# Kernel optimization log

Hardware: AMD Instinct MI355X
Metric: run time of the kernel (lower is better)

Reference implementation:

```python
import jax, jax.numpy as jnp
import numpy as np

B, H, S, D = 1, 16, 2048, 64


def setup_inputs() -> dict:
    key = jax.random.key(0)
    kq, kk, kv, km = jax.random.split(key, 4)
    q = jax.random.normal(kq, (B, H, S, D), dtype=jnp.float32)
    k = jax.random.normal(kk, (B, H, S, D), dtype=jnp.float32)
    v = jax.random.normal(kv, (B, H, S, D), dtype=jnp.float32)
    omask = jax.random.uniform(km, (B, H, S, S), dtype=jnp.float32)
    return {"q": q, "k": k, "v": v, "omask": omask}


def reference(q, k, v, omask):
    # mask = omask / sqrt(rowsum(omask)), nan -> 0
    row_sum = jnp.sum(omask, axis=-1, keepdims=True)  # [B,H,S,1]
    decay_mask = jnp.nan_to_num(omask / jnp.sqrt(row_sum), nan=0.0)
    # retention = (q k^T) * mask  -> [B,H,S,S]
    retention = jnp.einsum("bhsd,bhtd->bhst", q, k) * decay_mask
    # normalize by |rowsum(retention)| clamped to >= 1 (detached in original)
    scale = jnp.clip(jnp.abs(jnp.sum(retention, axis=-1, keepdims=True)), 1.0, None)
    retention = retention / scale
    # output = retention @ v -> [B,H,S,D]
    return jnp.einsum("bhst,bhtd->bhsd", retention, v)
```

## Files before the change

kernel.cpp:

```cpp
#include <hip/hip_runtime.h>

#define H 16
#define S 2048
#define D 64
#define BM 64
#define BN 64
#define NT (S / BN)
#define KP 72

typedef __attribute__((ext_vector_type(8))) short bf16x8;
typedef __attribute__((ext_vector_type(4))) short short4v;
typedef __attribute__((ext_vector_type(4))) float fx4;

static __device__ __forceinline__ short f2bf(float x) {
    unsigned u = __float_as_uint(x);
    u += 0x7fffu + ((u >> 16) & 1u);
    return (short)(u >> 16);
}
static __device__ __forceinline__ float bf2f(short s) {
    return __uint_as_float(((unsigned)(unsigned short)s) << 16);
}

__global__ __launch_bounds__(256)
void ParallelRetention_origin_25374666785438_kernel(
    const float* __restrict__ q, const float* __restrict__ k,
    const float* __restrict__ v, const float* __restrict__ om,
    float* __restrict__ out)
{
    __shared__ short ldsKh[2][BN * KP];
    __shared__ short ldsKl[2][BN * KP];
    __shared__ short ldsVT[2][BN * KP];
    __shared__ short ldsP[4 * 16 * KP];

    const int tid  = threadIdx.x;
    const int wave = tid >> 6;
    const int lane = tid & 63;
    const int col  = lane & 15;
    const int quad = lane >> 4;
    const int t_base = (tid >> 4) << 2;
    const int d4     = (tid & 15) << 2;

    const int h  = blockIdx.x & 15;
    const int qb = blockIdx.x >> 4;
    const int row0 = qb * BM;

    const size_t headQK = (size_t)h * S * D;
    const size_t headM  = (size_t)h * S * S;

    bf16x8 qh[2], qlo[2];
    {
        const int s_row = row0 + wave * 16 + col;
        const float* qp = q + headQK + (size_t)s_row * D + quad * 8;
#pragma unroll
        for (int c = 0; c < 2; ++c) {
            fx4 a = *(const fx4*)(qp + c * 32);
            fx4 b = *(const fx4*)(qp + c * 32 + 4);
            float f[8] = {a[0],a[1],a[2],a[3],b[0],b[1],b[2],b[3]};
#pragma unroll
            for (int j = 0; j < 8; ++j) {
                short hi = f2bf(f[j]);
                qh[c][j]  = hi;
                qlo[c][j] = f2bf(f[j] - bf2f(hi));
            }
        }
    }

    fx4 U[4];
#pragma unroll
    for (int nt = 0; nt < 4; ++nt) { U[nt][0]=0.f; U[nt][1]=0.f; U[nt][2]=0.f; U[nt][3]=0.f; }
    float rs_acc[4] = {0.f, 0.f, 0.f, 0.f};
    float T_acc[4]  = {0.f, 0.f, 0.f, 0.f};
    float om0[16], om1[16];

    const float* kbase0 = k + headQK;
    const float* vbase0 = v + headQK;
    const float* ombase = om + headM + (size_t)(row0 + wave * 16) * S;

    auto load_kv = [&](int t0, fx4 (&kr)[4], fx4 (&vr)[4]) {
        const float* kb = kbase0 + (size_t)t0 * D;
        const float* vb = vbase0 + (size_t)t0 * D;
#pragma unroll
        for (int r = 0; r < 4; ++r) {
            kr[r] = *(const fx4*)(kb + (size_t)(t_base + r) * D + d4);
            vr[r] = *(const fx4*)(vb + (size_t)(t_base + r) * D + d4);
        }
    };
    auto load_om = [&](int t0, float (&o)[16]) {
        const float* omp = ombase + t0;
#pragma unroll
        for (int tn = 0; tn < 4; ++tn)
#pragma unroll
            for (int r = 0; r < 4; ++r)
                o[tn * 4 + r] = omp[(size_t)(quad * 4 + r) * S + tn * 16 + col];
    };
    auto stage_write = [&](const fx4 (&kr)[4], const fx4 (&vr)[4],
                           short* Kh, short* Kl, short* VT) {
#pragma unroll
        for (int r = 0; r < 4; ++r) {
            short4v h4, l4;
#pragma unroll
            for (int j = 0; j < 4; ++j) {
                short hi = f2bf(kr[r][j]);
                h4[j] = hi;
                l4[j] = f2bf(kr[r][j] - bf2f(hi));
            }
            *(short4v*)(&Kh[(t_base + r) * KP + d4]) = h4;
            *(short4v*)(&Kl[(t_base + r) * KP + d4]) = l4;
        }
#pragma unroll
        for (int j = 0; j < 4; ++j) {
            short4v p;
#pragma unroll
            for (int r = 0; r < 4; ++r) p[r] = f2bf(vr[r][j]);
            *(short4v*)(&VT[(d4 + j) * KP + t_base]) = p;
        }
    };
    auto compute = [&](const short* Kh, const short* Kl, const short* VT,
                       const float (&omc)[16]) {
#pragma unroll
        for (int tn = 0; tn < 4; ++tn) {
            const short* kph = &Kh[(tn * 16 + col) * KP + quad * 8];
            const short* kpl = &Kl[(tn * 16 + col) * KP + quad * 8];
            bf16x8 kh0 = *(const bf16x8*)(kph);
            bf16x8 kh1 = *(const bf16x8*)(kph + 32);
            bf16x8 kl0 = *(const bf16x8*)(kpl);
            bf16x8 kl1 = *(const bf16x8*)(kpl + 32);
            fx4 z; z[0]=0.f; z[1]=0.f; z[2]=0.f; z[3]=0.f;
            z = __builtin_amdgcn_mfma_f32_16x16x32_bf16(qh[0],  kh0, z, 0, 0, 0);
            z = __builtin_amdgcn_mfma_f32_16x16x32_bf16(qh[1],  kh1, z, 0, 0, 0);
            z = __builtin_amdgcn_mfma_f32_16x16x32_bf16(qh[0],  kl0, z, 0, 0, 0);
            z = __builtin_amdgcn_mfma_f32_16x16x32_bf16(qh[1],  kl1, z, 0, 0, 0);
            z = __builtin_amdgcn_mfma_f32_16x16x32_bf16(qlo[0], kh0, z, 0, 0, 0);
            z = __builtin_amdgcn_mfma_f32_16x16x32_bf16(qlo[1], kh1, z, 0, 0, 0);
#pragma unroll
            for (int r = 0; r < 4; ++r) {
                float m = omc[tn * 4 + r];
                float p = z[r] * m;
                rs_acc[r] += m;
                T_acc[r]  += p;
                ldsP[(wave * 16 + quad * 4 + r) * KP + tn * 16 + col] = f2bf(p);
            }
        }
#pragma unroll
        for (int kt = 0; kt < 2; ++kt) {
            bf16x8 pa = *(const bf16x8*)(&ldsP[(wave * 16 + col) * KP + kt * 32 + quad * 8]);
#pragma unroll
            for (int nt = 0; nt < 4; ++nt) {
                bf16x8 vb = *(const bf16x8*)(&VT[(nt * 16 + col) * KP + kt * 32 + quad * 8]);
                U[nt] = __builtin_amdgcn_mfma_f32_16x16x32_bf16(pa, vb, U[nt], 0, 0, 0);
            }
        }
    };

    {
        fx4 kr[4], vr[4];
        load_kv(0, kr, vr);
        load_om(0, om0);
        stage_write(kr, vr, ldsKh[0], ldsKl[0], ldsVT[0]);
    }

    for (int it2 = 0; it2 < NT; it2 += 2) {
        {
            __syncthreads();
            fx4 kr[4], vr[4];
            load_kv((it2 + 1) * BN, kr, vr);
            load_om((it2 + 1) * BN, om1);
            compute(ldsKh[0], ldsKl[0], ldsVT[0], om0);
            stage_write(kr, vr, ldsKh[1], ldsKl[1], ldsVT[1]);
        }
        {
            __syncthreads();
            const bool pf = (it2 + 2 < NT);
            fx4 kr[4], vr[4];
            if (pf) {
                load_kv((it2 + 2) * BN, kr, vr);
                load_om((it2 + 2) * BN, om0);
            }
            compute(ldsKh[1], ldsKl[1], ldsVT[1], om1);
            if (pf) stage_write(kr, vr, ldsKh[0], ldsKl[0], ldsVT[0]);
        }
    }

#pragma unroll
    for (int off = 1; off < 16; off <<= 1) {
#pragma unroll
        for (int r = 0; r < 4; ++r) {
            rs_acc[r] += __shfl_xor(rs_acc[r], off, 64);
            T_acc[r]  += __shfl_xor(T_acc[r], off, 64);
        }
    }
    float factor[4];
#pragma unroll
    for (int r = 0; r < 4; ++r) {
        float rs  = rs_acc[r];
        float inv = rs > 0.f ? rsqrtf(rs) : 0.f;
        float rowsum = T_acc[r] * inv;
        float sc = fabsf(rowsum);
        sc = sc < 1.f ? 1.f : sc;
        factor[r] = inv / sc;
    }
    float* op = out + headQK + (size_t)(row0 + wave * 16) * D;
#pragma unroll
    for (int r = 0; r < 4; ++r)
#pragma unroll
        for (int nt = 0; nt < 4; ++nt)
            op[(size_t)(quad * 4 + r) * D + nt * 16 + col] = U[nt][r] * factor[r];
}

extern "C" void kernel_launch(void* const* d_in, const int* in_sizes, int n_in,
                              void* d_out, int out_size, void* d_ws, size_t ws_size,
                              hipStream_t stream) {
    const float* q  = (const float*)d_in[0];
    const float* k  = (const float*)d_in[1];
    const float* v  = (const float*)d_in[2];
    const float* om = (const float*)d_in[3];
    float* out = (float*)d_out;
    (void)in_sizes; (void)n_in; (void)out_size; (void)d_ws; (void)ws_size;

    dim3 grid(H * (S / BM));
    dim3 block(256);
    hipLaunchKernelGGL(ParallelRetention_origin_25374666785438_kernel,
                       grid, block, 0, stream, q, k, v, om, out);
}
```

Before: 408.8 us.

## Precompute bf16 K split and transposed V once, stage via direct global-to-LDS loads

Adds a prep kernel that converts K into bf16 hi/lo parts and V into a transposed bf16 layout in workspace, once per head. The main kernel then stages these tiles straight into swizzled LDS with global_load_lds, so each of the 32 query blocks per head no longer repeats the conversion. It also swaps MFMA operand order so the omask loads become contiguous fx4 vectors and row reductions become per-lane scalars, and it requests two blocks per CU. The cost is an extra launch and workspace traffic, plus XOR-swizzled LDS indexing that has to be correct.

Measured after the change: 394.7 us. 1.04x faster.

```diff
diff --git a/kernel.cpp b/kernel.cpp
--- a/kernel.cpp
+++ b/kernel.cpp
@@ -6,7 +6,6 @@
 #define BM 64
 #define BN 64
 #define NT (S / BN)
-#define KP 72
 
 typedef __attribute__((ext_vector_type(8))) short bf16x8;
 typedef __attribute__((ext_vector_type(4))) short short4v;
@@ -20,25 +19,83 @@
 static __device__ __forceinline__ float bf2f(short s) {
     return __uint_as_float(((unsigned)(unsigned short)s) << 16);
 }
+static __device__ __forceinline__ void gl_lds16(const void* g, void* l) {
+    __builtin_amdgcn_global_load_lds(
+        (const __attribute__((address_space(1))) unsigned int*)g,
+        (__attribute__((address_space(3))) unsigned int*)l, 16, 0, 0);
+}
 
 __global__ __launch_bounds__(256)
+void ParallelRetention_prep_kernel(
+    const float* __restrict__ k, const float* __restrict__ v,
+    short* __restrict__ khi, short* __restrict__ klo, short* __restrict__ vt)
+{
+    __shared__ short lv[64 * 72];
+    const int tid = threadIdx.x;
+    const int h  = blockIdx.x & 15;
+    const int sb = blockIdx.x >> 4;
+    const int s0 = sb * 64;
+    const int t_base = (tid >> 4) << 2;
+    const int d4     = (tid & 15) << 2;
+    const size_t hoff = (size_t)h * S * D;
+
+    {
+        const float* kb = k + hoff + (size_t)(s0 + t_base) * D + d4;
+#pragma unroll
+        for (int r = 0; r < 4; ++r) {
+            fx4 kr = *(const fx4*)(kb + (size_t)r * D);
+            short4v h4, l4;
+#pragma unroll
+            for (int j = 0; j < 4; ++j) {
+                short hi = f2bf(kr[j]);
+                h4[j] = hi;
+                l4[j] = f2bf(kr[j] - bf2f(hi));
+            }
+            *(short4v*)(&khi[hoff + (size_t)(s0 + t_base + r) * D + d4]) = h4;
+            *(short4v*)(&klo[hoff + (size_t)(s0 + t_base + r) * D + d4]) = l4;
+        }
+    }
+    {
+        const float* vb = v + hoff + (size_t)(s0 + t_base) * D + d4;
+        fx4 vr[4];
+#pragma unroll
+        for (int r = 0; r < 4; ++r) vr[r] = *(const fx4*)(vb + (size_t)r * D);
+#pragma unroll
+        for (int j = 0; j < 4; ++j) {
+            short4v p;
+#pragma unroll
+            for (int r = 0; r < 4; ++r) p[r] = f2bf(vr[r][j]);
+            *(short4v*)(&lv[(d4 + j) * 72 + t_base]) = p;
+        }
+    }
+    __syncthreads();
+    {
+        const int d = tid >> 2;
+        const int c = tid & 3;
+        bf16x8 a = *(const bf16x8*)(&lv[d * 72 + c * 16]);
+        bf16x8 b = *(const bf16x8*)(&lv[d * 72 + c * 16 + 8]);
+        short* o = vt + (size_t)h * D * S + (size_t)d * S + s0 + c * 16;
+        *(bf16x8*)(o)     = a;
+        *(bf16x8*)(o + 8) = b;
+    }
+}
+
+__global__ __launch_bounds__(256, 2)
 void ParallelRetention_origin_25374666785438_kernel(
-    const float* __restrict__ q, const float* __restrict__ k,
-    const float* __restrict__ v, const float* __restrict__ om,
-    float* __restrict__ out)
+    const float* __restrict__ q, const float* __restrict__ om,
+    const short* __restrict__ khi, const short* __restrict__ klo,
+    const short* __restrict__ vt, float* __restrict__ out)
 {
-    __shared__ short ldsKh[2][BN * KP];
-    __shared__ short ldsKl[2][BN * KP];
-    __shared__ short ldsVT[2][BN * KP];
-    __shared__ short ldsP[4 * 16 * KP];
+    __shared__ short ldsKh[2][64 * 64];
+    __shared__ short ldsKl[2][64 * 64];
+    __shared__ short ldsVT[2][64 * 64];
+    __shared__ short ldsP[64 * 64];
 
     const int tid  = threadIdx.x;
     const int wave = tid >> 6;
     const int lane = tid & 63;
     const int col  = lane & 15;
     const int quad = lane >> 4;
-    const int t_base = (tid >> 4) << 2;
-    const int d4     = (tid & 15) << 2;
 
     const int h  = blockIdx.x & 15;
     const int qb = blockIdx.x >> 4;
@@ -68,143 +125,120 @@
     fx4 U[4];
 #pragma unroll
     for (int nt = 0; nt < 4; ++nt) { U[nt][0]=0.f; U[nt][1]=0.f; U[nt][2]=0.f; U[nt][3]=0.f; }
-    float rs_acc[4] = {0.f, 0.f, 0.f, 0.f};
-    float T_acc[4]  = {0.f, 0.f, 0.f, 0.f};
-    float om0[16], om1[16];
-
-    const float* kbase0 = k + headQK;
-    const float* vbase0 = v + headQK;
-    const float* ombase = om + headM + (size_t)(row0 + wave * 16) * S;
-
-    auto load_kv = [&](int t0, fx4 (&kr)[4], fx4 (&vr)[4]) {
-        const float* kb = kbase0 + (size_t)t0 * D;
-        const float* vb = vbase0 + (size_t)t0 * D;
-#pragma unroll
-        for (int r = 0; r < 4; ++r) {
-            kr[r] = *(const fx4*)(kb + (size_t)(t_base + r) * D + d4);
-            vr[r] = *(const fx4*)(vb + (size_t)(t_base + r) * D + d4);
+    float rs_acc = 0.f, T_acc = 0.f;
+
+    const int xq   = quad ^ (col & 3);
+    const int cx   = (col >> 2) & 1;
+    const int rdC0 = col * 64 + xq * 8 + cx * 32;
+    const int rdC1 = col * 64 + xq * 8 + (cx ^ 1) * 32;
+    const int prow   = wave * 16 + col;
+    const int pwBase = prow * 64 + (quad & 1) * 4 + (((quad >> 1) ^ (col & 1))) * 8;
+    const int pxor   = (col >> 1) & 3;
+    const int prC0   = prow * 64 + xq * 8 + cx * 32;
+    const int prC1   = prow * 64 + xq * 8 + (cx ^ 1) * 32;
+    const int rowl = lane >> 3;
+    const int swz8 = ((lane & 7) ^ rowl) * 8;
+    const int kSrcOff = rowl * 64 + swz8;
+    const int vSrcOff = rowl * 2048 + swz8;
+
+    const short* khiH = khi + headQK;
+    const short* kloH = klo + headQK;
+    const short* vtH  = vt + (size_t)h * D * S;
+    const float* omp0 = om + headM + (size_t)(row0 + wave * 16 + col) * S + quad * 4;
+
+    auto stage = [&](int t0, short* dKh, short* dKl, short* dVT) {
+        const short* ks = khiH + (size_t)t0 * 64 + kSrcOff;
+        const short* ls = kloH + (size_t)t0 * 64 + kSrcOff;
+        const short* vs = vtH + t0 + vSrcOff;
+#pragma unroll
+        for (int c = 0; c < 6; ++c) {
+            int id = wave * 6 + c;
+            int j  = id & 7;
+            int tile = id >> 3;
+            if (tile == 0)      gl_lds16(ks + j * 512, dKh + j * 512);
+            else if (tile == 1) gl_lds16(ls + j * 512, dKl + j * 512);
+            else                gl_lds16(vs + (size_t)j * 8 * 2048, dVT + j * 512);
         }
     };
-    auto load_om = [&](int t0, float (&o)[16]) {
-        const float* omp = ombase + t0;
+    auto load_om = [&](int t0, fx4 (&o)[4]) {
 #pragma unroll
         for (int tn = 0; tn < 4; ++tn)
-#pragma unroll
-            for (int r = 0; r < 4; ++r)
-                o[tn * 4 + r] = omp[(size_t)(quad * 4 + r) * S + tn * 16 + col];
-    };
-    auto stage_write = [&](const fx4 (&kr)[4], const fx4 (&vr)[4],
-                           short* Kh, short* Kl, short* VT) {
-#pragma unroll
-        for (int r = 0; r < 4; ++r) {
-            short4v h4, l4;
-#pragma unroll
-            for (int j = 0; j < 4; ++j) {
-                short hi = f2bf(kr[r][j]);
-                h4[j] = hi;
-                l4[j] = f2bf(kr[r][j] - bf2f(hi));
-            }
-            *(short4v*)(&Kh[(t_base + r) * KP + d4]) = h4;
-            *(short4v*)(&Kl[(t_base + r) * KP + d4]) = l4;
-        }
-#pragma unroll
-        for (int j = 0; j < 4; ++j) {
-            short4v p;
-#pragma unroll
-            for (int r = 0; r < 4; ++r) p[r] = f2bf(vr[r][j]);
-            *(short4v*)(&VT[(d4 + j) * KP + t_base]) = p;
-        }
+            o[tn] = *(const fx4*)(omp0 + t0 + tn * 16);
     };
     auto compute = [&](const short* Kh, const short* Kl, const short* VT,
-                       const float (&omc)[16]) {
+                       const fx4 (&omc)[4]) {
 #pragma unroll
         for (int tn = 0; tn < 4; ++tn) {
-            const short* kph = &Kh[(tn * 16 + col) * KP + quad * 8];
-            const short* kpl = &Kl[(tn * 16 + col) * KP + quad * 8];
-            bf16x8 kh0 = *(const bf16x8*)(kph);
-            bf16x8 kh1 = *(const bf16x8*)(kph + 32);
-            bf16x8 kl0 = *(const bf16x8*)(kpl);
-            bf16x8 kl1 = *(const bf16x8*)(kpl + 32);
+            bf16x8 kh0 = *(const bf16x8*)(&Kh[tn * 1024 + rdC0]);
+            bf16x8 kh1 = *(const bf16x8*)(&Kh[tn * 1024 + rdC1]);
+            bf16x8 kl0 = *(const bf16x8*)(&Kl[tn * 1024 + rdC0]);
+            bf16x8 kl1 = *(const bf16x8*)(&Kl[tn * 1024 + rdC1]);
             fx4 z; z[0]=0.f; z[1]=0.f; z[2]=0.f; z[3]=0.f;
-            z = __builtin_amdgcn_mfma_f32_16x16x32_bf16(qh[0],  kh0, z, 0, 0, 0);
-            z = __builtin_amdgcn_mfma_f32_16x16x32_bf16(qh[1],  kh1, z, 0, 0, 0);
-            z = __builtin_amdgcn_mfma_f32_16x16x32_bf16(qh[0],  kl0, z, 0, 0, 0);
-            z = __builtin_amdgcn_mfma_f32_16x16x32_bf16(qh[1],  kl1, z, 0, 0, 0);
-            z = __builtin_amdgcn_mfma_f32_16x16x32_bf16(qlo[0], kh0, z, 0, 0, 0);
-            z = __builtin_amdgcn_mfma_f32_16x16x32_bf16(qlo[1], kh1, z, 0, 0, 0);
+            z = __builtin_amdgcn_mfma_f32_16x16x32_bf16(kh0, qh[0],  z, 0, 0, 0);
+            z = __builtin_amdgcn_mfma_f32_16x16x32_bf16(kh1, qh[1],  z, 0, 0, 0);
+            z = __builtin_amdgcn_mfma_f32_16x16x32_bf16(kl0, qh[0],  z, 0, 0, 0);
+            z = __builtin_amdgcn_mfma_f32_16x16x32_bf16(kl1, qh[1],  z, 0, 0, 0);
+            z = __builtin_amdgcn_mfma_f32_16x16x32_bf16(kh0, qlo[0], z, 0, 0, 0);
+            z = __builtin_amdgcn_mfma_f32_16x16x32_bf16(kh1, qlo[1], z, 0, 0, 0);
+            short4v p4;
 #pragma unroll
             for (int r = 0; r < 4; ++r) {
-                float m = omc[tn * 4 + r];
+                float m = omc[tn][r];
                 float p = z[r] * m;
-                rs_acc[r] += m;
-                T_acc[r]  += p;
-                ldsP[(wave * 16 + quad * 4 + r) * KP + tn * 16 + col] = f2bf(p);
+                rs_acc += m;
+                T_acc  += p;
+                p4[r] = f2bf(p);
             }
-        }
-#pragma unroll
-        for (int kt = 0; kt < 2; ++kt) {
-            bf16x8 pa = *(const bf16x8*)(&ldsP[(wave * 16 + col) * KP + kt * 32 + quad * 8]);
-#pragma unroll
-            for (int nt = 0; nt < 4; ++nt) {
-                bf16x8 vb = *(const bf16x8*)(&VT[(nt * 16 + col) * KP + kt * 32 + quad * 8]);
-                U[nt] = __builtin_amdgcn_mfma_f32_16x16x32_bf16(pa, vb, U[nt], 0, 0, 0);
-            }
+            *(short4v*)(&ldsP[pwBase + ((tn ^ pxor) << 4)]) = p4;
+        }
+        bf16x8 pa0 = *(const bf16x8*)(&ldsP[prC0]);
+        bf16x8 pa1 = *(const bf16x8*)(&ldsP[prC1]);
+#pragma unroll
+        for (int nt = 0; nt < 4; ++nt) {
+            bf16x8 vb0 = *(const bf16x8*)(&VT[nt * 1024 + rdC0]);
+            bf16x8 vb1 = *(const bf16x8*)(&VT[nt * 1024 + rdC1]);
+            U[nt] = __builtin_amdgcn_mfma_f32_16x16x32_bf16(pa0, vb0, U[nt], 0, 0, 0);
+            U[nt] = __builtin_amdgcn_mfma_f32_16x16x32_bf16(pa1, vb1, U[nt], 0, 0, 0);
         }
     };
 
-    {
-        fx4 kr[4], vr[4];
-        load_kv(0, kr, vr);
-        load_om(0, om0);
-        stage_write(kr, vr, ldsKh[0], ldsKl[0], ldsVT[0]);
-    }
-
-    for (int it2 = 0; it2 < NT; it2 += 2) {
-        {
-            __syncthreads();
-            fx4 kr[4], vr[4];
-            load_kv((it2 + 1) * BN, kr, vr);
-            load_om((it2 + 1) * BN, om1);
-            compute(ldsKh[0], ldsKl[0], ldsVT[0], om0);
-            stage_write(kr, vr, ldsKh[1], ldsKl[1], ldsVT[1]);
-        }
-        {
-            __syncthreads();
-            const bool pf = (it2 + 2 < NT);
-            fx4 kr[4], vr[4];
-            if (pf) {
-                load_kv((it2 + 2) * BN, kr, vr);
-                load_om((it2 + 2) * BN, om0);
-            }
-            compute(ldsKh[1], ldsKl[1], ldsVT[1], om1);
-            if (pf) stage_write(kr, vr, ldsKh[0], ldsKl[0], ldsVT[0]);
-        }
-    }
-
-#pragma unroll
-    for (int off = 1; off < 16; off <<= 1) {
-#pragma unroll
-        for (int r = 0; r < 4; ++r) {
-            rs_acc[r] += __shfl_xor(rs_acc[r], off, 64);
-            T_acc[r]  += __shfl_xor(T_acc[r], off, 64);
-        }
-    }
-    float factor[4];
-#pragma unroll
-    for (int r = 0; r < 4; ++r) {
-        float rs  = rs_acc[r];
-        float inv = rs > 0.f ? rsqrtf(rs) : 0.f;
-        float rowsum = T_acc[r] * inv;
-        float sc = fabsf(rowsum);
-        sc = sc < 1.f ? 1.f : sc;
-        factor[r] = inv / sc;
-    }
+    fx4 omA[4], omB[4];
+    stage(0, &ldsKh[0][0], &ldsKl[0][0], &ldsVT[0][0]);
+    load_om(0, omA);
+
+    for (int t = 0; t < NT; t += 2) {
+        __syncthreads();
+        if (t + 1 < NT) {
+            stage((t + 1) * BN, &ldsKh[1][0], &ldsKl[1][0], &ldsVT[1][0]);
+            load_om((t + 1) * BN, omB);
+        }
+        compute(&ldsKh[0][0], &ldsKl[0][0], &ldsVT[0][0], omA);
+        __syncthreads();
+        if (t + 2 < NT) {
+            stage((t + 2) * BN, &ldsKh[0][0], &ldsKl[0][0], &ldsVT[0][0]);
+            load_om((t + 2) * BN, omA);
+        }
+        compute(&ldsKh[1][0], &ldsKl[1][0], &ldsVT[1][0], omB);
+    }
+
+    rs_acc += __shfl_xor(rs_acc, 16, 64);
+    rs_acc += __shfl_xor(rs_acc, 32, 64);
+    T_acc  += __shfl_xor(T_acc, 16, 64);
+    T_acc  += __shfl_xor(T_acc, 32, 64);
+    float inv = rs_acc > 0.f ? rsqrtf(rs_acc) : 0.f;
+    float rowsum = T_acc * inv;
+    float sc = fabsf(rowsum);
+    sc = sc < 1.f ? 1.f : sc;
+    float fac = inv / sc;
+    float f[4];
+#pragma unroll
+    for (int r = 0; r < 4; ++r) f[r] = __shfl(fac, quad * 4 + r, 64);
     float* op = out + headQK + (size_t)(row0 + wave * 16) * D;
 #pragma unroll
     for (int r = 0; r < 4; ++r)
 #pragma unroll
         for (int nt = 0; nt < 4; ++nt)
-            op[(size_t)(quad * 4 + r) * D + nt * 16 + col] = U[nt][r] * factor[r];
+            op[(size_t)(quad * 4 + r) * D + nt * 16 + col] = U[nt][r] * f[r];
 }
 
 extern "C" void kernel_launch(void* const* d_in, const int* in_sizes, int n_in,
@@ -215,10 +249,14 @@
     const float* v  = (const float*)d_in[2];
     const float* om = (const float*)d_in[3];
     float* out = (float*)d_out;
-    (void)in_sizes; (void)n_in; (void)out_size; (void)d_ws; (void)ws_size;
-
-    dim3 grid(H * (S / BM));
-    dim3 block(256);
+    (void)in_sizes; (void)n_in; (void)out_size; (void)ws_size;
+
+    short* khi = (short*)d_ws;
+    short* klo = khi + (size_t)H * S * D;
+    short* vt  = klo + (size_t)H * S * D;
+
+    hipLaunchKernelGGL(ParallelRetention_prep_kernel,
+                       dim3(H * (S / 64)), dim3(256), 0, stream, k, v, khi, klo, vt);
     hipLaunchKernelGGL(ParallelRetention_origin_25374666785438_kernel,
-                       grid, block, 0, stream, q, k, v, om, out);
-}
+                       dim3(H * (S / BM)), dim3(256), 0, stream, q, om, khi, klo, vt, out);
+}
```
